# Performance work log

Hardware: AMD Instinct MI355X
Metric: run time of the kernel (lower is better)

## Reference

```python
import jax, jax.numpy as jnp
import numpy as np

N = 100000
E = 1600000
C = 64          # hidden_channels
F_IN = 3
F_OUT = 3
N_MP = 2        # message-passing layers


def _lin(k, fan_in, fan_out):
    kw, kb = jax.random.split(k)
    bound = 1.0 / np.sqrt(fan_in)
    W = jax.random.uniform(kw, (fan_in, fan_out), jnp.float32, -bound, bound)
    b = jax.random.uniform(kb, (fan_out,), jnp.float32, -bound, bound)
    return W, b


def setup_inputs() -> dict:
    key = jax.random.key(0)
    ks = jax.random.split(key, 32)
    x = jax.random.normal(ks[0], (N, F_IN), jnp.float32)
    pos = jax.random.normal(ks[1], (N, 3), jnp.float32)
    edge_index = jax.random.randint(ks[2], (2, E), 0, N, jnp.int64)

    enc_W0, enc_b0 = _lin(ks[3], F_IN, C)
    enc_W1, enc_b1 = _lin(ks[4], C, C)
    dec_W0, dec_b0 = _lin(ks[5], C, C)
    dec_W1, dec_b1 = _lin(ks[6], C, F_OUT)

    # stacked params for the N_MP message-passing layers
    eW0, eb0, eW1, eb1 = [], [], [], []
    nW0, nb0, nW1, nb1 = [], [], [], []
    for i in range(N_MP):
        W, b = _lin(ks[7 + 4 * i], 3 * C + 3, C); eW0.append(W); eb0.append(b)
        W, b = _lin(ks[8 + 4 * i], C, C);         eW1.append(W); eb1.append(b)
        W, b = _lin(ks[9 + 4 * i], 2 * C, C);     nW0.append(W); nb0.append(b)
        W, b = _lin(ks[10 + 4 * i], C, C);        nW1.append(W); nb1.append(b)
    stack = lambda xs: jnp.stack(xs, axis=0)
    return {
        "x": x, "pos": pos, "edge_index": edge_index,
        "enc_W0": enc_W0, "enc_b0": enc_b0, "enc_W1": enc_W1, "enc_b1": enc_b1,
        "dec_W0": dec_W0, "dec_b0": dec_b0, "dec_W1": dec_W1, "dec_b1": dec_b1,
        "mp_eW0": stack(eW0), "mp_eb0": stack(eb0),
        "mp_eW1": stack(eW1), "mp_eb1": stack(eb1),
        "mp_nW0": stack(nW0), "mp_nb0": stack(nb0),
        "mp_nW1": stack(nW1), "mp_nb1": stack(nb1),
    }


def reference(x, pos, edge_index,
              enc_W0, enc_b0, enc_W1, enc_b1,
              dec_W0, dec_b0, dec_W1, dec_b1,
              mp_eW0, mp_eb0, mp_eW1, mp_eb1,
              mp_nW0, mp_nb0, mp_nW1, mp_nb1):
    act = jax.nn.elu
    src, dst = edge_index[0], edge_index[1]

    # node encoder (2-layer MLP, activation between layers only)
    h = act(x @ enc_W0 + enc_b0)
    h = h @ enc_W1 + enc_b1

    pos_diff = pos[src] - pos[dst]  # [E, 3], constant across MP layers

    for i in range(N_MP):
        x_nei = h[src]               # [E, C]
        x_own = h[dst]               # [E, C]
        ea = jnp.concatenate([x_nei, x_own, x_nei - x_own, pos_diff], axis=1)
        ea = act(ea @ mp_eW0[i] + mp_eb0[i])
        ea = ea @ mp_eW1[i] + mp_eb1[i]
        # EdgeAggregation(aggr='add'): scatter-add edge features to target nodes
        agg = jax.ops.segment_sum(ea, dst, num_segments=N)  # [N, C]
        u = jnp.concatenate([h, agg], axis=1)                # [N, 2C]
        u = act(u @ mp_nW0[i] + mp_nb0[i])
        u = u @ mp_nW1[i] + mp_nb1[i]
        h = h + u  # residual

    # node decoder
    out = act(h @ dec_W0 + dec_b0)
    out = out @ dec_W1 + dec_b1
    return out
```

## Files before the change

kernel.cpp:

```cpp
#include <hip/hip_runtime.h>
#include <hip/hip_bf16.h>

#define NN 100000
#define NE 1600000
#define NBKT 391
#define BCAP 4608

typedef __hip_bfloat16 bf16;
typedef unsigned short u16;
typedef unsigned int u32;
typedef short bshort8 __attribute__((ext_vector_type(8)));
typedef float f32x4 __attribute__((ext_vector_type(4)));

__device__ __forceinline__ float b2f_raw(u16 u) {
    unsigned int w = ((unsigned int)u) << 16;
    float f; __builtin_memcpy(&f, &w, 4); return f;
}
__device__ __forceinline__ float uplo(u32 u) {
    u32 w = u << 16; float f; __builtin_memcpy(&f, &w, 4); return f;
}
__device__ __forceinline__ float uphi(u32 u) {
    u32 w = u & 0xFFFF0000u; float f; __builtin_memcpy(&f, &w, 4); return f;
}
__device__ __forceinline__ u16 f2bu(float f) {
    bf16 h = __float2bfloat16(f); u16 u; __builtin_memcpy(&u, &h, 2); return u;
}
__device__ __forceinline__ float eluf(float x) { return x > 0.f ? x : __expf(x) - 1.f; }

#define OFF_ENC_W0 0
#define OFF_ENC_B0 192
#define OFF_ENC_W1 256
#define OFF_ENC_B1 4352
#define OFF_DEC_W0 4416
#define OFF_DEC_B0 8512
#define OFF_DEC_W1 8576
#define OFF_DEC_B1 8768
#define OFF_EW0    8832
#define OFF_EB0    33792
#define OFF_EW1    33920
#define OFF_EB1    42112
#define OFF_NW0    42240
#define OFF_NB0    58624
#define OFF_NW1    58752
#define OFF_NB1    66944
#define OFF_WF     67072
#define OFF_BFOLD  75264
#define WBLK_WORDS 75392

#define SWZ_V   12288
#define SWZ_N0  24576
#define SWZ_N1  45056
#define SWZ_DC  53248
#define SWZ_ENC 57344
#define SWZ_U16 61440

__global__ void probe_kernel(const u16* __restrict__ xr,
                             const unsigned int* __restrict__ er,
                             int* __restrict__ flags, int* __restrict__ gcursor) {
    int tid = threadIdx.x;
    gcursor[tid] = 0;
    if (tid >= 64) return;
    int lane = tid;
    int wild = 0, oddnz = 0;
#pragma unroll
    for (int k = 0; k < 4; ++k) {
        int e = (xr[lane + k * 64] >> 7) & 0xFF;
        if (e > 140 || (e < 90 && e != 0)) wild++;
    }
#pragma unroll
    for (int k = 0; k < 2; ++k)
        if (er[1 + 2 * (lane + k * 64)] != 0u) oddnz++;
#pragma unroll
    for (int off = 32; off; off >>= 1) {
        wild += __shfl_down(wild, off);
        oddnz += __shfl_down(oddnz, off);
    }
    if (lane == 0) { flags[0] = (wild > 16) ? 1 : 0; flags[1] = (oddnz < 8) ? 1 : 0; }
}

struct WPtrs { const void* p[16]; };

__global__ void canon_weights(WPtrs wp, float* __restrict__ wblk,
                              const int* __restrict__ flags) {
    const int offs[16] = {OFF_ENC_W0, OFF_ENC_B0, OFF_ENC_W1, OFF_ENC_B1,
                          OFF_DEC_W0, OFF_DEC_B0, OFF_DEC_W1, OFF_DEC_B1,
                          OFF_EW0, OFF_EB0, OFF_EW1, OFF_EB1,
                          OFF_NW0, OFF_NB0, OFF_NW1, OFF_NB1};
    const int ns[16]   = {192, 64, 4096, 64, 4096, 64, 192, 3,
                          24960, 128, 8192, 128, 16384, 128, 8192, 128};
    int t = blockIdx.y;
    int i = blockIdx.x * blockDim.x + threadIdx.x;
    if (i >= ns[t]) return;
    const void* s = wp.p[t];
    float v = flags[0] ? ((const float*)s)[i] : b2f_raw(((const u16*)s)[i]);
    wblk[offs[t] + i] = v;
}

__global__ void prep_wf(float* __restrict__ wblk) {
    int idx = blockIdx.x * 256 + threadIdx.x;
    if (idx < 8192) {
        int l = idx >> 12, r = idx & 4095, k = r >> 6, c = r & 63;
        const float* e1 = wblk + OFF_EW1 + l * 4096 + k * 64;
        const float* n0 = wblk + OFF_NW0 + l * 8192 + 64 * 64;
        float s = 0.f;
#pragma unroll 8
        for (int m = 0; m < 64; ++m) s += e1[m] * n0[m * 64 + c];
        wblk[OFF_WF + idx] = s;
    } else if (idx < 8320) {
        int i2 = idx - 8192;
        int l = i2 >> 6, c = i2 & 63;
        const float* b1 = wblk + OFF_EB1 + l * 64;
        const float* n0 = wblk + OFF_NW0 + l * 8192 + 64 * 64;
        float s = 0.f;
#pragma unroll 8
        for (int m = 0; m < 64; ++m) s += b1[m] * n0[m * 64 + c];
        wblk[OFF_BFOLD + i2] = s;
    }
}

__global__ void prep_swz(const float* __restrict__ wblk, u16* __restrict__ swz) {
    int t = blockIdx.x * 256 + threadIdx.x;
    if (t >= SWZ_U16) return;
    float v = 0.f;
    if (t < SWZ_N0) {
        int isV = (t >= SWZ_V);
        int t2 = isV ? t - SWZ_V : t;
        int l = t2 / 6144, r = t2 % 6144;
        int ks = r >> 11, nt = (r >> 9) & 3, lane = (r >> 3) & 63, j = r & 7;
        int k = ks * 32 + ((lane >> 4) & 3) * 8 + j;
        int n = nt * 16 + (lane & 15);
        const float* W = wblk + OFF_EW0 + l * 12480;
        if (k < 64)
            v = isV ? (W[(64 + k) * 64 + n] - W[(128 + k) * 64 + n])
                    : (W[k * 64 + n] + W[(128 + k) * 64 + n]);
        else if (k < 67) {
            v = W[(192 + (k - 64)) * 64 + n];
            if (isV) v = -v;
        }
    } else if (t < SWZ_N1) {
        int t2 = t - SWZ_N0;
        int l = t2 / 10240, r = t2 % 10240;
        int ks = r >> 11, nt = (r >> 9) & 3, lane = (r >> 3) & 63, j = r & 7;
        int k = ks * 32 + ((lane >> 4) & 3) * 8 + j;
        int n = nt * 16 + (lane & 15);
        if (k < 64)        v = wblk[OFF_NW0 + l * 8192 + k * 64 + n];
        else if (k < 128)  v = wblk[OFF_WF + l * 4096 + (k - 64) * 64 + n];
        else if (k == 128) v = wblk[OFF_BFOLD + l * 64 + n];
    } else if (t < SWZ_DC) {
        int t2 = t - SWZ_N1;
        int l = t2 / 4096, r = t2 % 4096;
        int ks = r >> 11, nt = (r >> 9) & 3, lane = (r >> 3) & 63, j = r & 7;
        int k = ks * 32 + ((lane >> 4) & 3) * 8 + j;
        int n = nt * 16 + (lane & 15);
        v = wblk[OFF_NW1 + l * 4096 + k * 64 + n];
    } else if (t < SWZ_ENC) {
        int r = t - SWZ_DC;
        int ks = r >> 11, nt = (r >> 9) & 3, lane = (r >> 3) & 63, j = r & 7;
        int k = ks * 32 + ((lane >> 4) & 3) * 8 + j;
        int n = nt * 16 + (lane & 15);
        v = wblk[OFF_DEC_W0 + k * 64 + n];
    } else {
        int r = t - SWZ_ENC;
        int ks = r >> 11, nt = (r >> 9) & 3, lane = (r >> 3) & 63, j = r & 7;
        int k = ks * 32 + ((lane >> 4) & 3) * 8 + j;
        int n = nt * 16 + (lane & 15);
        v = wblk[OFF_ENC_W1 + k * 64 + n];
    }
    swz[t] = f2bu(v);
}


__global__ __launch_bounds__(1024) void passA_bin(
    const void* __restrict__ eiraw, const int* __restrict__ flags,
    u32* __restrict__ epk_b, int* __restrict__ gcursor) {
    __shared__ int hist[NBKT];
    __shared__ int binstart[NBKT];
    __shared__ int gbase_l[NBKT];
    __shared__ int fill[NBKT];
    __shared__ int sc[512];
    __shared__ u32 stage[4096];
    __shared__ u16 slotbin[4096];
    int tid = threadIdx.x;
    for (int i = tid; i < NBKT; i += 1024) hist[i] = 0;
    __syncthreads();
    int base = blockIdx.x * 4096;
    int total = NE - base; if (total > 4096) total = 4096;
    bool i64 = flags[1] != 0;
    u32 ed[4]; int bn[4];
#pragma unroll
    for (int k = 0; k < 4; ++k) {
        int e = base + tid + k * 1024;
        bn[k] = -1;
        if (e < NE) {
            int s, d;
            if (i64) {
                s = (int)((const long long*)eiraw)[e];
                d = (int)((const long long*)eiraw)[(size_t)NE + e];
            } else {
                s = ((const int*)eiraw)[e];
                d = ((const int*)eiraw)[(size_t)NE + e];
            }
            if ((unsigned)s >= NN) s = 0;
            if ((unsigned)d >= NN) d = 0;
            ed[k] = (u32)s | ((u32)(d & 255) << 17);
            bn[k] = d >> 8;
            atomicAdd(&hist[bn[k]], 1);
        }
    }
    __syncthreads();
    if (tid < 512) sc[tid] = (tid < NBKT) ? hist[tid] : 0;
    __syncthreads();
    for (int d = 1; d < 512; d <<= 1) {
        int v = (tid >= d && tid < 512) ? sc[tid - d] : 0;
        __syncthreads();
        if (tid < 512) sc[tid] += v;
        __syncthreads();
    }
    if (tid < NBKT) {
        binstart[tid] = sc[tid] - hist[tid];
        fill[tid] = 0;
        gbase_l[tid] = hist[tid] ? atomicAdd(&gcursor[tid], hist[tid]) : 0;
    }
    __syncthreads();
#pragma unroll
    for (int k = 0; k < 4; ++k) {
        if (bn[k] >= 0) {
            int p = binstart[bn[k]] + atomicAdd(&fill[bn[k]], 1);
            stage[p] = ed[k];
            slotbin[p] = (u16)bn[k];
        }
    }
    __syncthreads();
    for (int i = tid; i < total; i += 1024) {
        int b = slotbin[i];
        int gp = gbase_l[b] + (i - binstart[b]);
        if (gp < BCAP) epk_b[(size_t)b * BCAP + gp] = stage[i];
    }
}

__global__ __launch_bounds__(512) void scan391(const int* __restrict__ gcursor,
                                               int* __restrict__ gbase2) {
    __shared__ int s[512];
    int t = threadIdx.x;
    int v = 0;
    if (t < NBKT) { v = gcursor[t]; if (v > BCAP) v = BCAP; }
    s[t] = v;
    __syncthreads();
    for (int d = 1; d < 512; d <<= 1) {
        int u = (t >= d) ? s[t - d] : 0;
        __syncthreads();
        s[t] += u;
        __syncthreads();
    }
    if (t < NBKT) gbase2[t] = s[t] - v;
}

__global__ __launch_bounds__(1024) void passB_sort(
    const u32* __restrict__ epk_b, const int* __restrict__ gcursor,
    const int* __restrict__ gbase2, int* __restrict__ srcs,
    int* __restrict__ start) {
    __shared__ int h256[256];
    __shared__ int off256[256];
    __shared__ int sc[256];
    __shared__ u32 stage[BCAP];
    int b = blockIdx.x, tid = threadIdx.x;
    int cnt = gcursor[b]; if (cnt > BCAP) cnt = BCAP;
    for (int i = tid; i < 256; i += 1024) h256[i] = 0;
    __syncthreads();
    u32 ed[5]; int dl[5];
#pragma unroll
    for (int k = 0; k < 5; ++k) {
        int i = tid + k * 1024;
        dl[k] = -1;
        if (i < cnt) {
            ed[k] = epk_b[(size_t)b * BCAP + i];
            dl[k] = (int)(ed[k] >> 17);
            atomicAdd(&h256[dl[k]], 1);
        }
    }
    __syncthreads();
    if (tid < 256) sc[tid] = h256[tid];
    __syncthreads();
    for (int d = 1; d < 256; d <<= 1) {
        int v = (tid >= d && tid < 256) ? sc[tid - d] : 0;
        __syncthreads();
        if (tid < 256) sc[tid] += v;
        __syncthreads();
    }
    int gb = gbase2[b];
    if (tid < 256) {
        off256[tid] = sc[tid] - h256[tid];
        start[b * 256 + tid] = gb + sc[tid] - h256[tid];
    }
    __syncthreads();
#pragma unroll
    for (int k = 0; k < 5; ++k) {
        if (dl[k] >= 0) {
            int p = atomicAdd(&off256[dl[k]], 1);
            stage[p] = ed[k];
        }
    }
    __syncthreads();
    for (int i = tid; i < cnt; i += 1024) srcs[gb + i] = (int)(stage[i] & 0x1FFFFu);
}

__global__ __launch_bounds__(256) void encoder_mfma(
    const void* __restrict__ xraw, const void* __restrict__ praw,
    const float* __restrict__ wblk, const u16* __restrict__ swzE,
    float* __restrict__ h, u16* __restrict__ pos4b,
    const int* __restrict__ flags) {
    __shared__ __attribute__((aligned(16))) u16 sE[4096];
    int tid = threadIdx.x;
    for (int i = tid; i < 512; i += 256) ((uint4*)sE)[i] = ((const uint4*)swzE)[i];
    __syncthreads();
    int wid = tid >> 6, lane = tid & 63;
    int m16 = lane & 15, half = lane >> 4;
    int g = blockIdx.x * 4 + wid;
    if (g >= NN / 16) return;
    int n0 = g * 16 + m16;
    bool isf = flags[0] != 0;
    float x0, x1, x2;
    if (isf) {
        x0 = ((const float*)xraw)[n0 * 3 + 0];
        x1 = ((const float*)xraw)[n0 * 3 + 1];
        x2 = ((const float*)xraw)[n0 * 3 + 2];
    } else {
        x0 = b2f_raw(((const u16*)xraw)[n0 * 3 + 0]);
        x1 = b2f_raw(((const u16*)xraw)[n0 * 3 + 1]);
        x2 = b2f_raw(((const u16*)xraw)[n0 * 3 + 2]);
    }
    if (half == 0) {
        u16 pk[4]; pk[3] = 0;
#pragma unroll
        for (int c = 0; c < 3; ++c) {
            float pv = isf ? ((const float*)praw)[n0 * 3 + c]
                           : b2f_raw(((const u16*)praw)[n0 * 3 + c]);
            pk[c] = f2bu(pv);
        }
        *(ushort4*)(pos4b + (size_t)n0 * 4) = make_ushort4(pk[0], pk[1], pk[2], pk[3]);
    }
    const float* W0 = wblk + OFF_ENC_W0;
    const float* b0 = wblk + OFF_ENC_B0;
    bshort8 af0, af1;
#pragma unroll
    for (int j = 0; j < 8; ++j) {
        int c = half * 8 + j;
        float v = b0[c] + x0 * W0[c] + x1 * W0[64 + c] + x2 * W0[128 + c];
        af0[j] = (short)f2bu(eluf(v));
        int c2 = 32 + c;
        float v2 = b0[c2] + x0 * W0[c2] + x1 * W0[64 + c2] + x2 * W0[128 + c2];
        af1[j] = (short)f2bu(eluf(v2));
    }
    const bshort8* BE = (const bshort8*)sE;
    f32x4 acc[4];
#pragma unroll
    for (int nt = 0; nt < 4; ++nt) {
        float b = wblk[OFF_ENC_B1 + nt * 16 + m16];
        acc[nt] = f32x4{b, b, b, b};
    }
#pragma unroll
    for (int nt = 0; nt < 4; ++nt)
        acc[nt] = __builtin_amdgcn_mfma_f32_16x16x32_bf16(af0, BE[nt * 64 + lane], acc[nt], 0, 0, 0);
#pragma unroll
    for (int nt = 0; nt < 4; ++nt)
        acc[nt] = __builtin_amdgcn_mfma_f32_16x16x32_bf16(af1, BE[(4 + nt) * 64 + lane], acc[nt], 0, 0, 0);
#pragma unroll
    for (int nt = 0; nt < 4; ++nt)
#pragma unroll
        for (int r = 0; r < 4; ++r) {
            size_t ix = (size_t)(g * 16 + half * 4 + r) * 64 + nt * 16 + m16;
            h[ix] = acc[nt][r];
        }
}

__global__ __launch_bounds__(256) void uv_mfma(
    const float* __restrict__ h, const u16* __restrict__ pos4b,
    const u16* __restrict__ swzU, const u16* __restrict__ swzV,
    const float* __restrict__ eb0p,
    u16* __restrict__ U, u16* __restrict__ V) {
    __shared__ __attribute__((aligned(16))) u16 sU[6144];
    __shared__ __attribute__((aligned(16))) u16 sV[6144];
    int tid = threadIdx.x;
    for (int i = tid; i < 768; i += 256) {
        ((uint4*)sU)[i] = ((const uint4*)swzU)[i];
        ((uint4*)sV)[i] = ((const uint4*)swzV)[i];
    }
    __syncthreads();
    int wid = tid >> 6, lane = tid & 63;
    int m16 = lane & 15, half = lane >> 4;
    int g = blockIdx.x * 4 + wid;
    if (g >= NN / 16) return;
    int n0 = g * 16 + m16;
    const bshort8* BU = (const bshort8*)sU;
    const bshort8* BV = (const bshort8*)sV;
    bshort8 af0, af1, af2;
    {
        f32x4 a = *(const f32x4*)(h + (size_t)n0 * 64 + half * 8);
        f32x4 b = *(const f32x4*)(h + (size_t)n0 * 64 + half * 8 + 4);
        f32x4 c = *(const f32x4*)(h + (size_t)n0 * 64 + 32 + half * 8);
        f32x4 d = *(const f32x4*)(h + (size_t)n0 * 64 + 32 + half * 8 + 4);
#pragma unroll
        for (int j = 0; j < 4; ++j) {
            af0[j] = (short)f2bu(a[j]); af0[4 + j] = (short)f2bu(b[j]);
            af1[j] = (short)f2bu(c[j]); af1[4 + j] = (short)f2bu(d[j]);
            af2[j] = 0; af2[4 + j] = 0;
        }
        if (half == 0) {
            const u16* pp = pos4b + (size_t)n0 * 4;
            af2[0] = (short)pp[0]; af2[1] = (short)pp[1]; af2[2] = (short)pp[2];
        }
    }
    f32x4 aU[4], aV[4];
#pragma unroll
    for (int nt = 0; nt < 4; ++nt) {
        float bv = eb0p[nt * 16 + m16];
        aU[nt] = f32x4{0.f, 0.f, 0.f, 0.f};
        aV[nt] = f32x4{bv, bv, bv, bv};
    }
#pragma unroll
    for (int nt = 0; nt < 4; ++nt) {
        aU[nt] = __builtin_amdgcn_mfma_f32_16x16x32_bf16(af0, BU[nt * 64 + lane], aU[nt], 0, 0, 0);
        aV[nt] = __builtin_amdgcn_mfma_f32_16x16x32_bf16(af0, BV[nt * 64 + lane], aV[nt], 0, 0, 0);
    }
#pragma unroll
    for (int nt = 0; nt < 4; ++nt) {
        aU[nt] = __builtin_amdgcn_mfma_f32_16x16x32_bf16(af1, BU[(4 + nt) * 64 + lane], aU[nt], 0, 0, 0);
        aV[nt] = __builtin_amdgcn_mfma_f32_16x16x32_bf16(af1, BV[(4 + nt) * 64 + lane], aV[nt], 0, 0, 0);
    }
#pragma unroll
    for (int nt = 0; nt < 4; ++nt) {
        aU[nt] = __builtin_amdgcn_mfma_f32_16x16x32_bf16(af2, BU[(8 + nt) * 64 + lane], aU[nt], 0, 0, 0);
        aV[nt] = __builtin_amdgcn_mfma_f32_16x16x32_bf16(af2, BV[(8 + nt) * 64 + lane], aV[nt], 0, 0, 0);
    }
#pragma unroll
    for (int nt = 0; nt < 4; ++nt)
#pragma unroll
        for (int r = 0; r < 4; ++r) {
            size_t ix = (size_t)(g * 16 + half * 4 + r) * 64 + nt * 16 + m16;
            U[ix] = f2bu(aU[nt][r]);
            V[ix] = f2bu(aV[nt][r]);
        }
}

__global__ __launch_bounds__(256) void edge_sum(
    const u32* __restrict__ U32, const u32* __restrict__ V32,
    const int* __restrict__ srcs, const int* __restrict__ start,
    float* __restrict__ S, int totalwaves) {
    int tid = threadIdx.x;
    int w = blockIdx.x * 4 + (tid >> 6);
    int lane = tid & 63;
    int half = lane >> 5, t = lane & 31;
    int nb = (int)((long long)w * NN / totalwaves);
    int ne = (int)((long long)(w + 1) * NN / totalwaves);
    for (int n = nb; n < ne; ++n) {
        int s0 = start[n], s1 = start[n + 1];
        float aLo = 0.f, aHi = 0.f;
        if (s1 > s0) {
            u32 vv = V32[(size_t)n * 32 + t];
            float vlo = uplo(vv), vhi = uphi(vv);
            int eb = s0;
            while (eb + 8 <= s1) {
                int sv[4];
#pragma unroll
                for (int k = 0; k < 4; ++k) sv[k] = srcs[eb + half + 2 * k];
                u32 ug[4];
#pragma unroll
                for (int k = 0; k < 4; ++k) ug[k] = U32[(size_t)sv[k] * 32 + t];
#pragma unroll
                for (int k = 0; k < 4; ++k) {
                    aLo += eluf(uplo(ug[k]) + vlo);
                    aHi += eluf(uphi(ug[k]) + vhi);
                }
                eb += 8;
            }
            for (int e = eb + half; e < s1; e += 2) {
                u32 u = U32[(size_t)srcs[e] * 32 + t];
                aLo += eluf(uplo(u) + vlo);
                aHi += eluf(uphi(u) + vhi);
            }
            aLo += __shfl_xor(aLo, 32);
            aHi += __shfl_xor(aHi, 32);
        }
        if (half == 0)
            ((float2*)S)[(size_t)n * 32 + t] = make_float2(aLo, aHi);
    }
}

__global__ __launch_bounds__(256) void node_mfma(
    float* __restrict__ h, const float* __restrict__ S,
    const int* __restrict__ start, const float* __restrict__ wblk,
    const u16* __restrict__ swz, int l, int last,
    void* __restrict__ out, const int* __restrict__ flags) {
    __shared__ __attribute__((aligned(16))) u16 sN0[10240];
    __shared__ __attribute__((aligned(16))) u16 sN1[4096];
    __shared__ __attribute__((aligned(16))) u16 sDec[4096];
    __shared__ __attribute__((aligned(16))) float sT[4][1048];
    int tid = threadIdx.x;
    {
        const uint4* s0 = (const uint4*)(swz + SWZ_N0 + l * 10240);
        const uint4* s1 = (const uint4*)(swz + SWZ_N1 + l * 4096);
        const uint4* sd = (const uint4*)(swz + SWZ_DC);
        for (int i = tid; i < 1280; i += 256) ((uint4*)sN0)[i] = s0[i];
        for (int i = tid; i < 512; i += 256)  ((uint4*)sN1)[i] = s1[i];
        if (last)
            for (int i = tid; i < 512; i += 256) ((uint4*)sDec)[i] = sd[i];
    }
    __syncthreads();
    int wid = tid >> 6, lane = tid & 63;
    int m16 = lane & 15, half = lane >> 4;
    int g = blockIdx.x * 4 + wid;
    if (g >= NN / 16) return;
    int n0 = g * 16 + m16;
    const float* b0 = wblk + OFF_NB0 + l * 64;
    const float* b1 = wblk + OFF_NB1 + l * 64;
    const bshort8* B0 = (const bshort8*)sN0;
    const bshort8* B1 = (const bshort8*)sN1;
    const bshort8* BD = (const bshort8*)sDec;
    u16* myP = (u16*)sT[wid];
    float* sD = sT[wid];

    bshort8 afh0, afh1, afs0, afs1, afd;
    {
        f32x4 a = *(const f32x4*)(h + (size_t)n0 * 64 + half * 8);
        f32x4 b = *(const f32x4*)(h + (size_t)n0 * 64 + half * 8 + 4);
        f32x4 c = *(const f32x4*)(h + (size_t)n0 * 64 + 32 + half * 8);
        f32x4 d = *(const f32x4*)(h + (size_t)n0 * 64 + 32 + half * 8 + 4);
        f32x4 e = *(const f32x4*)(S + (size_t)n0 * 64 + half * 8);
        f32x4 f = *(const f32x4*)(S + (size_t)n0 * 64 + half * 8 + 4);
        f32x4 gg = *(const f32x4*)(S + (size_t)n0 * 64 + 32 + half * 8);
        f32x4 hh = *(const f32x4*)(S + (size_t)n0 * 64 + 32 + half * 8 + 4);
#pragma unroll
        for (int j = 0; j < 4; ++j) {
            afh0[j] = (short)f2bu(a[j]); afh0[4 + j] = (short)f2bu(b[j]);
            afh1[j] = (short)f2bu(c[j]); afh1[4 + j] = (short)f2bu(d[j]);
            afs0[j] = (short)f2bu(e[j]); afs0[4 + j] = (short)f2bu(f[j]);
            afs1[j] = (short)f2bu(gg[j]); afs1[4 + j] = (short)f2bu(hh[j]);
            afd[j] = 0; afd[4 + j] = 0;
        }
        if (half == 0) {
            float deg = (float)(start[n0 + 1] - start[n0]);
            afd[0] = (short)f2bu(deg);
        }
    }
    f32x4 acc[4];
#pragma unroll
    for (int nt = 0; nt < 4; ++nt) {
        float b = b0[nt * 16 + m16];
        acc[nt] = f32x4{b, b, b, b};
    }
#pragma unroll
    for (int nt = 0; nt < 4; ++nt)
        acc[nt] = __builtin_amdgcn_mfma_f32_16x16x32_bf16(afh0, B0[nt * 64 + lane], acc[nt], 0, 0, 0);
#pragma unroll
    for (int nt = 0; nt < 4; ++nt)
        acc[nt] = __builtin_amdgcn_mfma_f32_16x16x32_bf16(afh1, B0[(4 + nt) * 64 + lane], acc[nt], 0, 0, 0);
#pragma unroll
    for (int nt = 0; nt < 4; ++nt)
        acc[nt] = __builtin_amdgcn_mfma_f32_16x16x32_bf16(afs0, B0[(8 + nt) * 64 + lane], acc[nt], 0, 0, 0);
#pragma unroll
    for (int nt = 0; nt < 4; ++nt)
        acc[nt] = __builtin_amdgcn_mfma_f32_16x16x32_bf16(afs1, B0[(12 + nt) * 64 + lane], acc[nt], 0, 0, 0);
#pragma unroll
    for (int nt = 0; nt < 4; ++nt)
        acc[nt] = __builtin_amdgcn_mfma_f32_16x16x32_bf16(afd, B0[(16 + nt) * 64 + lane], acc[nt], 0, 0, 0);
#pragma unroll
    for (int nt = 0; nt < 4; ++nt)
#pragma unroll
        for (int r = 0; r < 4; ++r) {
            float v = acc[nt][r];
            v = eluf(v);
            myP[(half * 4 + r) * 72 + nt * 16 + m16] = f2bu(v);
        }
    f32x4 acc2[4];
#pragma unroll
    for (int nt = 0; nt < 4; ++nt) {
        float b = b1[nt * 16 + m16];
        acc2[nt] = f32x4{b, b, b, b};
    }
#pragma unroll
    for (int ks = 0; ks < 2; ++ks) {
        bshort8 av = *(const bshort8*)(myP + m16 * 72 + ks * 32 + half * 8);
#pragma unroll
        for (int nt = 0; nt < 4; ++nt)
            acc2[nt] = __builtin_amdgcn_mfma_f32_16x16x32_bf16(
                av, B1[(ks * 4 + nt) * 64 + lane], acc2[nt], 0, 0, 0);
    }
    float nh[4][4];
#pragma unroll
    for (int nt = 0; nt < 4; ++nt)
#pragma unroll
        for (int r = 0; r < 4; ++r) {
            size_t ix = (size_t)(g * 16 + half * 4 + r) * 64 + nt * 16 + m16;
            nh[nt][r] = h[ix] + acc2[nt][r];
        }
    if (!last) {
#pragma unroll
        for (int nt = 0; nt < 4; ++nt)
#pragma unroll
            for (int r = 0; r < 4; ++r) {
                size_t ix = (size_t)(g * 16 + half * 4 + r) * 64 + nt * 16 + m16;
                h[ix] = nh[nt][r];
            }
        return;
    }
#pragma unroll
    for (int nt = 0; nt < 4; ++nt)
#pragma unroll
        for (int r = 0; r < 4; ++r)
            myP[(half * 4 + r) * 72 + nt * 16 + m16] = f2bu(nh[nt][r]);
    const float* db0 = wblk + OFF_DEC_B0;
    f32x4 acc3[4];
#pragma unroll
    for (int nt = 0; nt < 4; ++nt) {
        float b = db0[nt * 16 + m16];
        acc3[nt] = f32x4{b, b, b, b};
    }
#pragma unroll
    for (int ks = 0; ks < 2; ++ks) {
        bshort8 av = *(const bshort8*)(myP + m16 * 72 + ks * 32 + half * 8);
#pragma unroll
        for (int nt = 0; nt < 4; ++nt)
            acc3[nt] = __builtin_amdgcn_mfma_f32_16x16x32_bf16(
                av, BD[(ks * 4 + nt) * 64 + lane], acc3[nt], 0, 0, 0);
    }
#pragma unroll
    for (int nt = 0; nt < 4; ++nt)
#pragma unroll
        for (int r = 0; r < 4; ++r) {
            float v = acc3[nt][r];
            v = eluf(v);
            sD[(half * 4 + r) * 65 + nt * 16 + m16] = v;
        }
    if (lane < 48) {
        int j = lane / 3, o = lane - j * 3;
        const float* dW1 = wblk + OFF_DEC_W1;
        float oacc = wblk[OFF_DEC_B1 + o];
#pragma unroll
        for (int k = 0; k < 64; ++k) oacc += sD[j * 65 + k] * dW1[k * 3 + o];
        int nn = g * 16 + j;
        if (flags[0]) ((float*)out)[nn * 3 + o] = oacc;
        else          ((bf16*)out)[nn * 3 + o] = __float2bfloat16(oacc);
    }
}

extern "C" void kernel_launch(void* const* d_in, const int* in_sizes, int n_in,
                              void* d_out, int out_size, void* d_ws, size_t ws_size,
                              hipStream_t stream) {
    int*   flags   = (int*)d_ws;
    float* wblk    = (float*)d_ws + 16;
    u16*   swz     = (u16*)(wblk + WBLK_WORDS);
    u16*   pos4b   = swz + SWZ_U16;
    int*   gcursor = (int*)(pos4b + 400000);
    int*   gbase2  = gcursor + 512;
    int*   start   = gbase2 + 512;
    int*   srcs    = start + NN + 512;
    float* S       = (float*)(srcs + NE);
    float* hbuf    = S + (size_t)NN * 64;
    u16*   U       = (u16*)(hbuf + (size_t)NN * 64);
    u16*   V       = U + (size_t)NN * 64;
    u32*   epk_b   = (u32*)S;

    probe_kernel<<<1, 512, 0, stream>>>((const u16*)d_in[0],
                                        (const unsigned int*)d_in[2], flags, gcursor);

    WPtrs wp;
    wp.p[0] = d_in[3];  wp.p[1] = d_in[4];  wp.p[2] = d_in[5];  wp.p[3] = d_in[6];
    wp.p[4] = d_in[7];  wp.p[5] = d_in[8];  wp.p[6] = d_in[9];  wp.p[7] = d_in[10];
    wp.p[8] = d_in[11]; wp.p[9] = d_in[12]; wp.p[10] = d_in[13]; wp.p[11] = d_in[14];
    wp.p[12] = d_in[15]; wp.p[13] = d_in[16]; wp.p[14] = d_in[17]; wp.p[15] = d_in[18];
    canon_weights<<<dim3(98, 16), 256, 0, stream>>>(wp, wblk, flags);
    prep_wf<<<33, 256, 0, stream>>>(wblk);
    prep_swz<<<240, 256, 0, stream>>>(wblk, swz);

    passA_bin<<<(NE + 4095) / 4096, 1024, 0, stream>>>(d_in[2], flags, epk_b, gcursor);
    scan391<<<1, 512, 0, stream>>>(gcursor, gbase2);
    passB_sort<<<NBKT, 1024, 0, stream>>>(epk_b, gcursor, gbase2, srcs, start);

    const int NODE_BLOCKS = (NN / 16 + 3) / 4;
    encoder_mfma<<<NODE_BLOCKS, 256, 0, stream>>>(
        d_in[0], d_in[1], wblk, swz + SWZ_ENC, hbuf, pos4b, flags);

    const int EDGE_BLOCKS = 2048;
    const int TOTALWAVES = EDGE_BLOCKS * 4;
    for (int l = 0; l < 2; ++l) {
        uv_mfma<<<NODE_BLOCKS, 256, 0, stream>>>(
            hbuf, pos4b, swz + (size_t)l * 6144, swz + SWZ_V + (size_t)l * 6144,
            wblk + OFF_EB0 + l * 64, U, V);
        edge_sum<<<EDGE_BLOCKS, 256, 0, stream>>>(
            (const u32*)U, (const u32*)V, srcs, start, S, TOTALWAVES);
        node_mfma<<<NODE_BLOCKS, 256, 0, stream>>>(
            hbuf, S, start, wblk, swz, l, (l == 1), d_out, flags);
    }
}
```

Measured before the change: 334.2 us.

## Split U/V/S into four 16-channel chunks for cache-local edge gathers

```diff
diff --git a/kernel.cpp b/kernel.cpp
--- a/kernel.cpp
+++ b/kernel.cpp
@@ -169,7 +169,6 @@
     swz[t] = f2bu(v);
 }
 
-
 __global__ __launch_bounds__(1024) void passA_bin(
     const void* __restrict__ eiraw, const int* __restrict__ flags,
     u32* __restrict__ epk_b, int* __restrict__ gcursor) {
@@ -436,7 +435,7 @@
     for (int nt = 0; nt < 4; ++nt)
 #pragma unroll
         for (int r = 0; r < 4; ++r) {
-            size_t ix = (size_t)(g * 16 + half * 4 + r) * 64 + nt * 16 + m16;
+            size_t ix = (size_t)nt * NN * 16 + (size_t)(g * 16 + half * 4 + r) * 16 + m16;
             U[ix] = f2bu(aU[nt][r]);
             V[ix] = f2bu(aV[nt][r]);
         }
@@ -445,44 +444,38 @@
 __global__ __launch_bounds__(256) void edge_sum(
     const u32* __restrict__ U32, const u32* __restrict__ V32,
     const int* __restrict__ srcs, const int* __restrict__ start,
-    float* __restrict__ S, int totalwaves) {
+    float* __restrict__ S, int wavesPerChunk) {
     int tid = threadIdx.x;
-    int w = blockIdx.x * 4 + (tid >> 6);
+    int bid = blockIdx.x;
+    int c = (bid >> 1) & 3;
+    int local = (bid >> 3) * 2 + (bid & 1);
+    int w = local * 4 + (tid >> 6);
     int lane = tid & 63;
-    int half = lane >> 5, t = lane & 31;
-    int nb = (int)((long long)w * NN / totalwaves);
-    int ne = (int)((long long)(w + 1) * NN / totalwaves);
+    int e3 = lane >> 3, t = lane & 7;
+    const u32* Uc = U32 + (size_t)c * NN * 8;
+    const u32* Vc = V32 + (size_t)c * NN * 8;
+    float* Sc = S + (size_t)c * NN * 16;
+    int nb = (int)((long long)w * NN / wavesPerChunk);
+    int ne = (int)((long long)(w + 1) * NN / wavesPerChunk);
     for (int n = nb; n < ne; ++n) {
         int s0 = start[n], s1 = start[n + 1];
         float aLo = 0.f, aHi = 0.f;
-        if (s1 > s0) {
-            u32 vv = V32[(size_t)n * 32 + t];
-            float vlo = uplo(vv), vhi = uphi(vv);
-            int eb = s0;
-            while (eb + 8 <= s1) {
-                int sv[4];
-#pragma unroll
-                for (int k = 0; k < 4; ++k) sv[k] = srcs[eb + half + 2 * k];
-                u32 ug[4];
-#pragma unroll
-                for (int k = 0; k < 4; ++k) ug[k] = U32[(size_t)sv[k] * 32 + t];
-#pragma unroll
-                for (int k = 0; k < 4; ++k) {
-                    aLo += eluf(uplo(ug[k]) + vlo);
-                    aHi += eluf(uphi(ug[k]) + vhi);
-                }
-                eb += 8;
+        for (int eb = s0; eb < s1; eb += 8) {
+            int e = eb + e3;
+            bool valid = e < s1;
+            int sv = valid ? srcs[e] : 0;
+            u32 ug = Uc[(size_t)sv * 8 + t];
+            u32 vv = Vc[(size_t)n * 8 + t];
+            if (valid) {
+                aLo += eluf(uplo(ug) + uplo(vv));
+                aHi += eluf(uphi(ug) + uphi(vv));
             }
-            for (int e = eb + half; e < s1; e += 2) {
-                u32 u = U32[(size_t)srcs[e] * 32 + t];
-                aLo += eluf(uplo(u) + vlo);
-                aHi += eluf(uphi(u) + vhi);
-            }
-            aLo += __shfl_xor(aLo, 32);
-            aHi += __shfl_xor(aHi, 32);
-        }
-        if (half == 0)
-            ((float2*)S)[(size_t)n * 32 + t] = make_float2(aLo, aHi);
+        }
+        aLo += __shfl_xor(aLo, 8);  aHi += __shfl_xor(aHi, 8);
+        aLo += __shfl_xor(aLo, 16); aHi += __shfl_xor(aHi, 16);
+        aLo += __shfl_xor(aLo, 32); aHi += __shfl_xor(aHi, 32);
+        if (e3 == 0)
+            ((float2*)Sc)[(size_t)n * 8 + t] = make_float2(aLo, aHi);
     }
 }
 
@@ -525,10 +518,13 @@
         f32x4 b = *(const f32x4*)(h + (size_t)n0 * 64 + half * 8 + 4);
         f32x4 c = *(const f32x4*)(h + (size_t)n0 * 64 + 32 + half * 8);
         f32x4 d = *(const f32x4*)(h + (size_t)n0 * 64 + 32 + half * 8 + 4);
-        f32x4 e = *(const f32x4*)(S + (size_t)n0 * 64 + half * 8);
-        f32x4 f = *(const f32x4*)(S + (size_t)n0 * 64 + half * 8 + 4);
-        f32x4 gg = *(const f32x4*)(S + (size_t)n0 * 64 + 32 + half * 8);
-        f32x4 hh = *(const f32x4*)(S + (size_t)n0 * 64 + 32 + half * 8 + 4);
+        int c0 = half >> 1, off0 = (half & 1) * 8;
+        const float* Sp0 = S + (size_t)c0 * NN * 16 + (size_t)n0 * 16 + off0;
+        const float* Sp1 = S + (size_t)(2 + c0) * NN * 16 + (size_t)n0 * 16 + off0;
+        f32x4 e = *(const f32x4*)(Sp0);
+        f32x4 f = *(const f32x4*)(Sp0 + 4);
+        f32x4 gg = *(const f32x4*)(Sp1);
+        f32x4 hh = *(const f32x4*)(Sp1 + 4);
 #pragma unroll
         for (int j = 0; j < 4; ++j) {
             afh0[j] = (short)f2bu(a[j]); afh0[4 + j] = (short)f2bu(b[j]);
@@ -681,13 +677,13 @@
         d_in[0], d_in[1], wblk, swz + SWZ_ENC, hbuf, pos4b, flags);
 
     const int EDGE_BLOCKS = 2048;
-    const int TOTALWAVES = EDGE_BLOCKS * 4;
+    const int WAVES_PER_CHUNK = (EDGE_BLOCKS / 4) * 4;
     for (int l = 0; l < 2; ++l) {
         uv_mfma<<<NODE_BLOCKS, 256, 0, stream>>>(
             hbuf, pos4b, swz + (size_t)l * 6144, swz + SWZ_V + (size_t)l * 6144,
             wblk + OFF_EB0 + l * 64, U, V);
         edge_sum<<<EDGE_BLOCKS, 256, 0, stream>>>(
-            (const u32*)U, (const u32*)V, srcs, start, S, TOTALWAVES);
+            (const u32*)U, (const u32*)V, srcs, start, S, WAVES_PER_CHUNK);
         node_mfma<<<NODE_BLOCKS, 256, 0, stream>>>(
             hbuf, S, start, wblk, swz, l, (l == 1), d_out, flags);
     }
```

Result: slower. 422.3 us (+26.4%).
